# Kernel optimization log

Measured on AMD Instinct MI355X. Metric: run time of the kernel, lower is better.

The kernel has to match this reference:

```python
import jax, jax.numpy as jnp
import numpy as np

T = 4096
INPUT_SIZE = 64
DIMS = 64          # __init__ forces dimensions = input_size
RESERVOIR = 2048
OUTPUT_SIZE = 1
SPECTRAL_RADIUS = 0.95


def setup_inputs() -> dict:
    key = jax.random.key(0)
    k_x, k_c, k_in, k_res, k_w, k_b = jax.random.split(key, 6)
    X = jax.random.normal(k_x, (T, INPUT_SIZE, 1), dtype=jnp.float32)
    # conversion matrix: random then QR -> orthonormal columns
    C_raw = jax.random.uniform(k_c, (DIMS, INPUT_SIZE), dtype=jnp.float32)
    C, _ = jnp.linalg.qr(C_raw)
    # ESN weights. W_res entries ~ N(0, 1/RESERVOIR): circular-law spectral
    # radius ~= 1, scaled to the target spectral radius.
    W_in = jax.random.uniform(k_in, (RESERVOIR, DIMS), dtype=jnp.float32, minval=-1.0, maxval=1.0)
    W_res = jax.random.normal(k_res, (RESERVOIR, RESERVOIR), dtype=jnp.float32) * (SPECTRAL_RADIUS / np.sqrt(RESERVOIR))
    dense_W = jax.random.normal(k_w, (OUTPUT_SIZE, RESERVOIR + DIMS), dtype=jnp.float32) * 0.02
    dense_b = jnp.zeros((OUTPUT_SIZE,), dtype=jnp.float32)
    return {"X": X, "C": C, "W_in": W_in, "W_res": W_res,
            "dense_W": dense_W, "dense_b": dense_b}


def reference(X, C, W_in, W_res, dense_W, dense_b):
    # project all inputs up front: u_t = C @ x_t   -> (T, DIMS)
    U = jnp.einsum('di,tio->tdo', C, X)[..., 0]
    # sequential reservoir recurrence: h_t = tanh(W_in u_t + W_res h_{t-1})
    def step(h, u):
        h_new = jnp.tanh(W_in @ u + W_res @ h)
        return h_new, h_new
    h0 = jnp.zeros((W_res.shape[0],), dtype=X.dtype)
    _, H = jax.lax.scan(step, h0, U)            # (T, RESERVOIR)
    # ESN forward returns vstack(u, h); dense1 reads its transpose
    feats = jnp.concatenate([U, H], axis=1)     # (T, DIMS + RESERVOIR)
    y = feats @ dense_W.T + dense_b             # (T, OUTPUT_SIZE)
    # torch: stack of (1, OUTPUT) rows -> (T,1,OUT), permute(0,2,1) -> (T,OUT,1)
    return y[:, :, None]
```

## Files before the change

kernel.cpp:

```cpp
#include <hip/hip_runtime.h>

#define TT 4096

typedef __attribute__((ext_vector_type(2))) unsigned int u2v;
typedef __attribute__((ext_vector_type(4))) unsigned int u4v;
typedef __attribute__((ext_vector_type(2))) __fp16 f16x2;
typedef __attribute__((ext_vector_type(2))) _Float16 F16x2;
union HU { unsigned int u; f16x2 hf; F16x2 hF; };


__global__ void esn_prep(const float* __restrict__ C,
                         const float* __restrict__ Win,
                         const float* __restrict__ dW,
                         float* __restrict__ M,
                         float* __restrict__ wtil) {
  __shared__ float s[64];
  const int b = blockIdx.x, i = threadIdx.x;
  if (b < 2048) {
    s[i] = Win[b * 64 + i];
    __syncthreads();
    float acc = 0.f;
#pragma unroll 16
    for (int d = 0; d < 64; ++d) acc += s[d] * C[d * 64 + i];
    M[b * 64 + i] = acc;
  } else {
    s[i] = dW[i];
    __syncthreads();
    float acc = 0.f;
    for (int d = 0; d < 64; ++d) acc += s[d] * C[d * 64 + i];
    wtil[i] = acc;
  }
}

__device__ __forceinline__ float fast_tanh(float x) {
  const float e = __builtin_amdgcn_exp2f(x * 2.8853900817779268f);
  return 1.0f - 2.0f * __builtin_amdgcn_rcpf(e + 1.0f);
}

__device__ __forceinline__ float fdot2f(const HU a, const HU b, float c) {
#if __has_builtin(__builtin_amdgcn_fdot2)
  return __builtin_amdgcn_fdot2(a.hF, b.hF, c, false);
#else
  return c + (float)a.hf.x * (float)b.hf.x + (float)a.hf.y * (float)b.hf.y;
#endif
}

__global__ __launch_bounds__(1024) void esn_recur(
    const float* __restrict__ X, const float* __restrict__ M,
    const float* __restrict__ W, const float* __restrict__ dW,
    unsigned int* __restrict__ hpub, float* __restrict__ yp) {
  extern __shared__ unsigned int smem[];
  unsigned int* w16 = smem;
  unsigned int* shh = smem + 32768;
  unsigned int* pub = smem + 33792;
  float* psm = (float*)(smem + 33808);
  const int tid = threadIdx.x;
  const int lane = tid & 63;
  const int wave = tid >> 6;
  const int b = blockIdx.x;
  const int r0 = b * 32 + wave * 2;
  const float m0 = M[r0 * 64 + lane];
  const float m1 = M[(r0 + 1) * 64 + lane];
  const float dw0 = dW[64 + r0];
  const float dw1 = dW[64 + r0 + 1];
  for (int i = tid; i < 32768; i += 1024) {
    const int r = i >> 10, j = i & 1023;
    const float2 w2 = *(const float2*)(W + (size_t)(b * 32 + r) * 2048 + 2 * j);
    HU hu; hu.hf = __builtin_amdgcn_cvt_pkrtz(w2.x, w2.y);
    w16[i] = hu.u;
  }
  if (tid < 1024) shh[tid] = 0u;
  __syncthreads();

  for (int t = 0; t < TT; ++t) {
    const float xv = X[t * 64 + lane];
    float a0 = m0 * xv, a1 = m1 * xv;
    const unsigned int* wr0 = w16 + ((wave * 2) << 10);
    const unsigned int* wr1 = wr0 + 1024;
#pragma unroll
    for (int j = 0; j < 4; ++j) {
      const int o = 4 * lane + 256 * j;
      const u4v hv = *(const u4v*)(shh + o);
      const u4v wv0 = *(const u4v*)(wr0 + o);
      const u4v wv1 = *(const u4v*)(wr1 + o);
#pragma unroll
      for (int k = 0; k < 4; ++k) {
        HU ha, wa, wb;
        ha.u = hv[k]; wa.u = wv0[k]; wb.u = wv1[k];
        a0 = fdot2f(wa, ha, a0);
        a1 = fdot2f(wb, ha, a1);
      }
    }
#pragma unroll
    for (int off = 32; off; off >>= 1) {
      a0 += __shfl_xor(a0, off, 64);
      a1 += __shfl_xor(a1, off, 64);
    }
    if (lane == 0) {
      const float h0 = fast_tanh(a0);
      const float h1 = fast_tanh(a1);
      HU pk; pk.hf = __builtin_amdgcn_cvt_pkrtz(h0, h1);
      pub[wave] = pk.u;
      psm[wave] = dw0 * h0 + dw1 * h1;
    }
    __syncthreads();
    const unsigned tg = (unsigned)t + 1u;
    if (wave == 0) {
      if (t + 1 < TT) {
        unsigned int* slot = hpub + ((t & 1) << 11);
        if (tid < 16) {
          u2v pv; pv.x = pub[tid]; pv.y = tg;
          asm volatile("global_store_dwordx2 %0, %1, off sc0 sc1"
                       :: "v"(slot + 2 * (16 * b + tid)), "v"(pv) : "memory");
        }
        const unsigned int* b0 = slot + 2 * lane;
        const unsigned int* b1 = b0 + 1024;
        u2v q0, q1, q2, q3, q4, q5, q6, q7, q8, q9, qa, qb, qc, qd, qe, qf;
        for (;;) {
          asm volatile(
              "global_load_dwordx2 %0, %16, off sc0 sc1\n\t"
              "global_load_dwordx2 %1, %16, off offset:512 sc0 sc1\n\t"
              "global_load_dwordx2 %2, %16, off offset:1024 sc0 sc1\n\t"
              "global_load_dwordx2 %3, %16, off offset:1536 sc0 sc1\n\t"
              "global_load_dwordx2 %4, %16, off offset:2048 sc0 sc1\n\t"
              "global_load_dwordx2 %5, %16, off offset:2560 sc0 sc1\n\t"
              "global_load_dwordx2 %6, %16, off offset:3072 sc0 sc1\n\t"
              "global_load_dwordx2 %7, %16, off offset:3584 sc0 sc1\n\t"
              "global_load_dwordx2 %8, %17, off sc0 sc1\n\t"
              "global_load_dwordx2 %9, %17, off offset:512 sc0 sc1\n\t"
              "global_load_dwordx2 %10, %17, off offset:1024 sc0 sc1\n\t"
              "global_load_dwordx2 %11, %17, off offset:1536 sc0 sc1\n\t"
              "global_load_dwordx2 %12, %17, off offset:2048 sc0 sc1\n\t"
              "global_load_dwordx2 %13, %17, off offset:2560 sc0 sc1\n\t"
              "global_load_dwordx2 %14, %17, off offset:3072 sc0 sc1\n\t"
              "global_load_dwordx2 %15, %17, off offset:3584 sc0 sc1\n\t"
              "s_waitcnt vmcnt(0)"
              : "=&v"(q0), "=&v"(q1), "=&v"(q2), "=&v"(q3),
                "=&v"(q4), "=&v"(q5), "=&v"(q6), "=&v"(q7),
                "=&v"(q8), "=&v"(q9), "=&v"(qa), "=&v"(qb),
                "=&v"(qc), "=&v"(qd), "=&v"(qe), "=&v"(qf)
              : "v"(b0), "v"(b1)
              : "memory");
          bool ok = (q0.y == tg) && (q1.y == tg) && (q2.y == tg) &&
                    (q3.y == tg) && (q4.y == tg) && (q5.y == tg) &&
                    (q6.y == tg) && (q7.y == tg) && (q8.y == tg) &&
                    (q9.y == tg) && (qa.y == tg) && (qb.y == tg) &&
                    (qc.y == tg) && (qd.y == tg) && (qe.y == tg) &&
                    (qf.y == tg);
          if (__all(ok)) break;
        }
        shh[lane] = q0.x;          shh[64 + lane] = q1.x;
        shh[128 + lane] = q2.x;    shh[192 + lane] = q3.x;
        shh[256 + lane] = q4.x;    shh[320 + lane] = q5.x;
        shh[384 + lane] = q6.x;    shh[448 + lane] = q7.x;
        shh[512 + lane] = q8.x;    shh[576 + lane] = q9.x;
        shh[640 + lane] = qa.x;    shh[704 + lane] = qb.x;
        shh[768 + lane] = qc.x;    shh[832 + lane] = qd.x;
        shh[896 + lane] = qe.x;    shh[960 + lane] = qf.x;
      }
    } else if (tid == 64) {
      float s = 0.f;
#pragma unroll
      for (int wv = 0; wv < 16; ++wv) s += psm[wv];
      yp[t * 64 + b] = s;
    }
    __syncthreads();
  }
}

__global__ void esn_out(const float* __restrict__ X,
                        const float* __restrict__ wtil,
                        const float* __restrict__ yp,
                        const float* __restrict__ bptr,
                        float* __restrict__ out) {
  const int tid = threadIdx.x;
  const int lane = tid & 63;
  const int wave = tid >> 6;
  const int t = blockIdx.x * 4 + wave;
  float v = wtil[lane] * X[t * 64 + lane] + yp[t * 64 + lane];
#pragma unroll
  for (int off = 32; off; off >>= 1) v += __shfl_xor(v, off, 64);
  if (lane == 0) out[t] = v + bptr[0];
}

#define ESN_LDS_BYTES 135296

struct EsnInit {
  EsnInit() {
    (void)hipFuncSetAttribute(reinterpret_cast<const void*>(&esn_recur),
                              hipFuncAttributeMaxDynamicSharedMemorySize,
                              ESN_LDS_BYTES);
  }
};
static EsnInit g_esn_init;

extern "C" void kernel_launch(void* const* d_in, const int* in_sizes, int n_in,
                              void* d_out, int out_size, void* d_ws, size_t ws_size,
                              hipStream_t stream) {
  const float* X   = (const float*)d_in[0];
  const float* C   = (const float*)d_in[1];
  const float* Win = (const float*)d_in[2];
  const float* W   = (const float*)d_in[3];
  const float* dW  = (const float*)d_in[4];
  const float* db  = (const float*)d_in[5];
  float* ws   = (float*)d_ws;
  float* M    = ws;
  float* wtil = ws + 131072;
  float* yp   = ws + 131200;
  unsigned int* hpub = (unsigned int*)(ws + 393344);

  esn_prep<<<2049, 64, 0, stream>>>(C, Win, dW, M, wtil);

  void* args[] = {(void*)&X, (void*)&M, (void*)&W, (void*)&dW,
                  (void*)&hpub, (void*)&yp};
  (void)hipLaunchCooperativeKernel(reinterpret_cast<void*>(&esn_recur), dim3(64),
                                   dim3(1024), args, ESN_LDS_BYTES, stream);

  esn_out<<<1024, 256, 0, stream>>>(X, wtil, yp, db, (float*)d_out);
}
```

Measured before the change: 10.65 ms.

## Spread cross-block hidden-state polling across all threads with double-buffered LDS

Each wave's lane 0 now publishes its packed hidden pair to global memory directly, with no intermediate LDS staging. All 1024 threads then each poll a single slot of the published hidden vector, where before one wave issued 16 loads per lane in a loop. The shared hidden buffer is double-buffered, which removes the second __syncthreads per step, and the next X value is prefetched. The per-step partial output sum is deferred by one step. In exchange every thread spins on global memory, which raises L2 polling traffic.

Result: slower. 13.31 ms (+24.9%).

```diff
diff --git a/kernel.cpp b/kernel.cpp
--- a/kernel.cpp
+++ b/kernel.cpp
@@ -52,8 +52,7 @@
   extern __shared__ unsigned int smem[];
   unsigned int* w16 = smem;
   unsigned int* shh = smem + 32768;
-  unsigned int* pub = smem + 33792;
-  float* psm = (float*)(smem + 33808);
+  float* psm = (float*)(smem + 34816);
   const int tid = threadIdx.x;
   const int lane = tid & 63;
   const int wave = tid >> 6;
@@ -69,18 +68,23 @@
     HU hu; hu.hf = __builtin_amdgcn_cvt_pkrtz(w2.x, w2.y);
     w16[i] = hu.u;
   }
-  if (tid < 1024) shh[tid] = 0u;
+  shh[tid] = 0u;
   __syncthreads();
 
+  const int pown = ((tid >> 4) == b);
+  const unsigned int* wr0 = w16 + ((wave * 2) << 10);
+  const unsigned int* wr1 = wr0 + 1024;
+  float xv = X[lane];
+
   for (int t = 0; t < TT; ++t) {
-    const float xv = X[t * 64 + lane];
+    const int cur = t & 1;
+    const unsigned int* shc = shh + (cur << 10);
+    unsigned int* shn = shh + ((cur ^ 1) << 10);
     float a0 = m0 * xv, a1 = m1 * xv;
-    const unsigned int* wr0 = w16 + ((wave * 2) << 10);
-    const unsigned int* wr1 = wr0 + 1024;
 #pragma unroll
     for (int j = 0; j < 4; ++j) {
       const int o = 4 * lane + 256 * j;
-      const u4v hv = *(const u4v*)(shh + o);
+      const u4v hv = *(const u4v*)(shc + o);
       const u4v wv0 = *(const u4v*)(wr0 + o);
       const u4v wv1 = *(const u4v*)(wr1 + o);
 #pragma unroll
@@ -96,75 +100,45 @@
       a0 += __shfl_xor(a0, off, 64);
       a1 += __shfl_xor(a1, off, 64);
     }
+    const unsigned tg = (unsigned)t + 1u;
+    unsigned int* slot = hpub + ((t & 1) << 11);
+    const int tn = (t + 1 < TT) ? t + 1 : t;
+    const float xnext = X[tn * 64 + lane];
     if (lane == 0) {
       const float h0 = fast_tanh(a0);
       const float h1 = fast_tanh(a1);
       HU pk; pk.hf = __builtin_amdgcn_cvt_pkrtz(h0, h1);
-      pub[wave] = pk.u;
-      psm[wave] = dw0 * h0 + dw1 * h1;
+      if (t + 1 < TT) {
+        u2v pv; pv.x = pk.u; pv.y = tg;
+        asm volatile("global_store_dwordx2 %0, %1, off sc0 sc1"
+                     :: "v"(slot + 2 * (16 * b + wave)), "v"(pv) : "memory");
+        shn[16 * b + wave] = pk.u;
+      }
+      psm[cur * 16 + wave] = dw0 * h0 + dw1 * h1;
+    }
+    if (t + 1 < TT && !pown) {
+      const unsigned int* ap = slot + 2 * tid;
+      u2v q;
+      do {
+        asm volatile("global_load_dwordx2 %0, %1, off sc0 sc1\n\t"
+                     "s_waitcnt vmcnt(0)"
+                     : "=&v"(q) : "v"(ap) : "memory");
+      } while (q.y != tg);
+      shn[tid] = q.x;
+    } else if (pown && tid == 16 * b + 1 && t > 0) {
+      float s = 0.f;
+#pragma unroll
+      for (int w = 0; w < 16; ++w) s += psm[((t - 1) & 1) * 16 + w];
+      yp[(t - 1) * 64 + b] = s;
     }
     __syncthreads();
-    const unsigned tg = (unsigned)t + 1u;
-    if (wave == 0) {
-      if (t + 1 < TT) {
-        unsigned int* slot = hpub + ((t & 1) << 11);
-        if (tid < 16) {
-          u2v pv; pv.x = pub[tid]; pv.y = tg;
-          asm volatile("global_store_dwordx2 %0, %1, off sc0 sc1"
-                       :: "v"(slot + 2 * (16 * b + tid)), "v"(pv) : "memory");
-        }
-        const unsigned int* b0 = slot + 2 * lane;
-        const unsigned int* b1 = b0 + 1024;
-        u2v q0, q1, q2, q3, q4, q5, q6, q7, q8, q9, qa, qb, qc, qd, qe, qf;
-        for (;;) {
-          asm volatile(
-              "global_load_dwordx2 %0, %16, off sc0 sc1\n\t"
-              "global_load_dwordx2 %1, %16, off offset:512 sc0 sc1\n\t"
-              "global_load_dwordx2 %2, %16, off offset:1024 sc0 sc1\n\t"
-              "global_load_dwordx2 %3, %16, off offset:1536 sc0 sc1\n\t"
-              "global_load_dwordx2 %4, %16, off offset:2048 sc0 sc1\n\t"
-              "global_load_dwordx2 %5, %16, off offset:2560 sc0 sc1\n\t"
-              "global_load_dwordx2 %6, %16, off offset:3072 sc0 sc1\n\t"
-              "global_load_dwordx2 %7, %16, off offset:3584 sc0 sc1\n\t"
-              "global_load_dwordx2 %8, %17, off sc0 sc1\n\t"
-              "global_load_dwordx2 %9, %17, off offset:512 sc0 sc1\n\t"
-              "global_load_dwordx2 %10, %17, off offset:1024 sc0 sc1\n\t"
-              "global_load_dwordx2 %11, %17, off offset:1536 sc0 sc1\n\t"
-              "global_load_dwordx2 %12, %17, off offset:2048 sc0 sc1\n\t"
-              "global_load_dwordx2 %13, %17, off offset:2560 sc0 sc1\n\t"
-              "global_load_dwordx2 %14, %17, off offset:3072 sc0 sc1\n\t"
-              "global_load_dwordx2 %15, %17, off offset:3584 sc0 sc1\n\t"
-              "s_waitcnt vmcnt(0)"
-              : "=&v"(q0), "=&v"(q1), "=&v"(q2), "=&v"(q3),
-                "=&v"(q4), "=&v"(q5), "=&v"(q6), "=&v"(q7),
-                "=&v"(q8), "=&v"(q9), "=&v"(qa), "=&v"(qb),
-                "=&v"(qc), "=&v"(qd), "=&v"(qe), "=&v"(qf)
-              : "v"(b0), "v"(b1)
-              : "memory");
-          bool ok = (q0.y == tg) && (q1.y == tg) && (q2.y == tg) &&
-                    (q3.y == tg) && (q4.y == tg) && (q5.y == tg) &&
-                    (q6.y == tg) && (q7.y == tg) && (q8.y == tg) &&
-                    (q9.y == tg) && (qa.y == tg) && (qb.y == tg) &&
-                    (qc.y == tg) && (qd.y == tg) && (qe.y == tg) &&
-                    (qf.y == tg);
-          if (__all(ok)) break;
-        }
-        shh[lane] = q0.x;          shh[64 + lane] = q1.x;
-        shh[128 + lane] = q2.x;    shh[192 + lane] = q3.x;
-        shh[256 + lane] = q4.x;    shh[320 + lane] = q5.x;
-        shh[384 + lane] = q6.x;    shh[448 + lane] = q7.x;
-        shh[512 + lane] = q8.x;    shh[576 + lane] = q9.x;
-        shh[640 + lane] = qa.x;    shh[704 + lane] = qb.x;
-        shh[768 + lane] = qc.x;    shh[832 + lane] = qd.x;
-        shh[896 + lane] = qe.x;    shh[960 + lane] = qf.x;
-      }
-    } else if (tid == 64) {
-      float s = 0.f;
+    xv = xnext;
+  }
+  if (tid == 16 * b + 1) {
+    float s = 0.f;
 #pragma unroll
-      for (int wv = 0; wv < 16; ++wv) s += psm[wv];
-      yp[t * 64 + b] = s;
-    }
-    __syncthreads();
+    for (int w = 0; w < 16; ++w) s += psm[((TT - 1) & 1) * 16 + w];
+    yp[(TT - 1) * 64 + b] = s;
   }
 }
 
@@ -183,7 +157,7 @@
   if (lane == 0) out[t] = v + bptr[0];
 }
 
-#define ESN_LDS_BYTES 135296
+#define ESN_LDS_BYTES 139392
 
 struct EsnInit {
   EsnInit() {
```

## Double-buffer LDS hidden state and publish per-wave to cut a block barrier

Applied to the files above, without the earlier changes.

Each wave now publishes its own packed h values directly to global memory, replicated across 8 copies so groups of blocks poll different regions. This removes the intermediate LDS publish and one __syncthreads per step. The hidden-state LDS buffer and the partial-sum buffer are double-buffered, so the output partial sum is written one step late and the next X value is prefetched early. The cost is more global store traffic and a larger LDS footprint.

After: 13.02 ms. +22.2%, slower.

```diff
diff --git a/kernel.cpp b/kernel.cpp
--- a/kernel.cpp
+++ b/kernel.cpp
@@ -52,8 +52,7 @@
   extern __shared__ unsigned int smem[];
   unsigned int* w16 = smem;
   unsigned int* shh = smem + 32768;
-  unsigned int* pub = smem + 33792;
-  float* psm = (float*)(smem + 33808);
+  float* psm = (float*)(smem + 34816);
   const int tid = threadIdx.x;
   const int lane = tid & 63;
   const int wave = tid >> 6;
@@ -69,18 +68,22 @@
     HU hu; hu.hf = __builtin_amdgcn_cvt_pkrtz(w2.x, w2.y);
     w16[i] = hu.u;
   }
-  if (tid < 1024) shh[tid] = 0u;
+  shh[tid] = 0u;
   __syncthreads();
 
+  const unsigned int* wr0 = w16 + ((wave * 2) << 10);
+  const unsigned int* wr1 = wr0 + 1024;
+  float xv = X[lane];
+
   for (int t = 0; t < TT; ++t) {
-    const float xv = X[t * 64 + lane];
+    const int cur = t & 1;
+    const unsigned int* shc = shh + (cur << 10);
+    unsigned int* shn = shh + ((cur ^ 1) << 10);
     float a0 = m0 * xv, a1 = m1 * xv;
-    const unsigned int* wr0 = w16 + ((wave * 2) << 10);
-    const unsigned int* wr1 = wr0 + 1024;
 #pragma unroll
     for (int j = 0; j < 4; ++j) {
       const int o = 4 * lane + 256 * j;
-      const u4v hv = *(const u4v*)(shh + o);
+      const u4v hv = *(const u4v*)(shc + o);
       const u4v wv0 = *(const u4v*)(wr0 + o);
       const u4v wv1 = *(const u4v*)(wr1 + o);
 #pragma unroll
@@ -96,24 +99,23 @@
       a0 += __shfl_xor(a0, off, 64);
       a1 += __shfl_xor(a1, off, 64);
     }
-    if (lane == 0) {
-      const float h0 = fast_tanh(a0);
-      const float h1 = fast_tanh(a1);
-      HU pk; pk.hf = __builtin_amdgcn_cvt_pkrtz(h0, h1);
-      pub[wave] = pk.u;
-      psm[wave] = dw0 * h0 + dw1 * h1;
-    }
-    __syncthreads();
     const unsigned tg = (unsigned)t + 1u;
+    unsigned int* par = hpub + ((t & 1) << 14);
+    const int tn = (t + 1 < TT) ? t + 1 : t;
+    const float xnext = X[tn * 64 + lane];
+    const float h0 = fast_tanh(a0);
+    const float h1 = fast_tanh(a1);
+    HU pk; pk.hf = __builtin_amdgcn_cvt_pkrtz(h0, h1);
+    if (t + 1 < TT && lane < 8) {
+      u2v pv; pv.x = pk.u; pv.y = tg;
+      unsigned int* dst = par + (lane << 11) + 2 * (16 * b + wave);
+      asm volatile("global_store_dwordx2 %0, %1, off sc0 sc1"
+                   :: "v"(dst), "v"(pv) : "memory");
+    }
+    if (lane == 0) psm[cur * 16 + wave] = dw0 * h0 + dw1 * h1;
     if (wave == 0) {
       if (t + 1 < TT) {
-        unsigned int* slot = hpub + ((t & 1) << 11);
-        if (tid < 16) {
-          u2v pv; pv.x = pub[tid]; pv.y = tg;
-          asm volatile("global_store_dwordx2 %0, %1, off sc0 sc1"
-                       :: "v"(slot + 2 * (16 * b + tid)), "v"(pv) : "memory");
-        }
-        const unsigned int* b0 = slot + 2 * lane;
+        const unsigned int* b0 = par + ((b >> 3) << 11) + 2 * lane;
         const unsigned int* b1 = b0 + 1024;
         u2v q0, q1, q2, q3, q4, q5, q6, q7, q8, q9, qa, qb, qc, qd, qe, qf;
         for (;;) {
@@ -149,22 +151,29 @@
                     (qf.y == tg);
           if (__all(ok)) break;
         }
-        shh[lane] = q0.x;          shh[64 + lane] = q1.x;
-        shh[128 + lane] = q2.x;    shh[192 + lane] = q3.x;
-        shh[256 + lane] = q4.x;    shh[320 + lane] = q5.x;
-        shh[384 + lane] = q6.x;    shh[448 + lane] = q7.x;
-        shh[512 + lane] = q8.x;    shh[576 + lane] = q9.x;
-        shh[640 + lane] = qa.x;    shh[704 + lane] = qb.x;
-        shh[768 + lane] = qc.x;    shh[832 + lane] = qd.x;
-        shh[896 + lane] = qe.x;    shh[960 + lane] = qf.x;
+        shn[lane] = q0.x;          shn[64 + lane] = q1.x;
+        shn[128 + lane] = q2.x;    shn[192 + lane] = q3.x;
+        shn[256 + lane] = q4.x;    shn[320 + lane] = q5.x;
+        shn[384 + lane] = q6.x;    shn[448 + lane] = q7.x;
+        shn[512 + lane] = q8.x;    shn[576 + lane] = q9.x;
+        shn[640 + lane] = qa.x;    shn[704 + lane] = qb.x;
+        shn[768 + lane] = qc.x;    shn[832 + lane] = qd.x;
+        shn[896 + lane] = qe.x;    shn[960 + lane] = qf.x;
       }
-    } else if (tid == 64) {
+    } else if (tid == 64 && t > 0) {
       float s = 0.f;
 #pragma unroll
-      for (int wv = 0; wv < 16; ++wv) s += psm[wv];
-      yp[t * 64 + b] = s;
+      for (int w = 0; w < 16; ++w) s += psm[((t - 1) & 1) * 16 + w];
+      yp[(t - 1) * 64 + b] = s;
     }
     __syncthreads();
+    xv = xnext;
+  }
+  if (tid == 64) {
+    float s = 0.f;
+#pragma unroll
+    for (int w = 0; w < 16; ++w) s += psm[((TT - 1) & 1) * 16 + w];
+    yp[(TT - 1) * 64 + b] = s;
   }
 }
 
@@ -183,7 +192,7 @@
   if (lane == 0) out[t] = v + bptr[0];
 }
 
-#define ESN_LDS_BYTES 135296
+#define ESN_LDS_BYTES 139392
 
 struct EsnInit {
   EsnInit() {
```
